# Optimization experiments

Measured on AMD Instinct MI355X. Metric: run time of the kernel, lower is better.

Reference implementation:

```python
import jax, jax.numpy as jnp
import numpy as np

EPS = 1e-5

def _ln(x, g, b):
    m = x.mean(-1, keepdims=True)
    v = jnp.var(x, axis=-1, keepdims=True)
    return (x - m) * jax.lax.rsqrt(v + EPS) * g + b

def _conv(x, w, b, stride=1, pad=1):
    y = jax.lax.conv_general_dilated(x, w, (stride, stride), [(pad, pad), (pad, pad)],
                                     dimension_numbers=('NCHW', 'OIHW', 'NCHW'))
    return y + b[None, :, None, None]

def _bn(x, g, b, m, v):
    # inference-mode BatchNorm2d
    inv = jax.lax.rsqrt(v + EPS)
    return (x - m[None, :, None, None]) * (g * inv)[None, :, None, None] + b[None, :, None, None]

def _sru_dir(u0, u1, u2, res, vf, vr, bf, br, reverse):
    # elementwise gated recurrence (SRU v2, identity activation, no dropout)
    def step(c, inp):
        a0, a1, a2, rx = inp
        f = jax.nn.sigmoid(a1 + vf * c + bf)
        c2 = f * c + (1.0 - f) * a0
        r = jax.nn.sigmoid(a2 + vr * c2 + br)
        return c2, r * c2 + (1.0 - r) * rx
    c0 = jnp.zeros_like(u0[0])
    _, hs = jax.lax.scan(step, c0, (u0, u1, u2, res), reverse=reverse)
    return hs

def _sru_layer(x, g, b, wp, w, vc, bias, k, h):
    # x: [L,B,n_in]; layer_norm on input, factored weight (projection), bidirectional
    xn = _ln(x, g, b)
    L, B, _ = xn.shape
    U = (xn @ wp) @ w                      # [L,B,2*k*h]
    U = U.reshape(L, B, 2, k, h)
    outs = []
    for d, rev in ((0, False), (1, True)):
        u = U[:, :, d]
        res = u[..., 3, :] if k == 4 else xn[..., d * h:(d + 1) * h]
        outs.append(_sru_dir(u[..., 0, :], u[..., 1, :], u[..., 2, :], res,
                             vc[d, 0], vc[d, 1], bias[d, 0], bias[d, 1], rev))
    return jnp.concatenate(outs, axis=-1)

def _forward(x, conv0_w, conv0_b, rconv1_w, rconv1_b, rbn1_g, rbn1_b, rbn1_m, rbn1_v,
             rconv2_w, rconv2_b, rbn2_g, rbn2_b, rbn2_m, rbn2_v,
             ln0_g, ln0_b, wproj0, w0, vc0, bias0, ln_g, ln_b, wproj, w, vc, bias,
             cln_g, cln_b, cls_w):
    H = 512
    h = _conv(x, conv0_w, conv0_b, stride=2)           # [B,32,F/2,T/2]
    for i in range(3):                                  # 3 residual blocks
        r = h
        h1 = jax.nn.relu(_bn(_conv(h, rconv1_w[i], rconv1_b[i]), rbn1_g[i], rbn1_b[i], rbn1_m[i], rbn1_v[i]))
        h2 = _bn(_conv(h1, rconv2_w[i], rconv2_b[i]), rbn2_g[i], rbn2_b[i], rbn2_m[i], rbn2_v[i])
        h = jax.nn.relu(h2 + r)
    Bb, C, Fr, Tt = h.shape
    s = h.reshape(Bb, C * Fr, Tt).transpose(2, 0, 1)   # [T,B,2048]
    s = _sru_layer(s, ln0_g, ln0_b, wproj0, w0, vc0, bias0, 4, H)  # layer 0: n_in != n_out -> k=4
    for i in range(3):                                  # layers 1..3: n_in == n_out -> k=3
        s = _sru_layer(s, ln_g[i], ln_b[i], wproj[i], w[i], vc[i], bias[i], 3, H)
    s = s.transpose(1, 0, 2)                            # [B,T,1024]
    s = _ln(s, cln_g, cln_b)
    return s @ cls_w                                    # [B,T,30]

def setup_inputs():
    key = jax.random.key(0)
    ks = iter(jax.random.split(key, 32))
    def nrm(shape, scale=1.0):
        return jax.random.normal(next(ks), shape, jnp.float32) * scale
    H, P, F2, D, hb = 512, 256, 2048, 1024, -2.0
    d = {}
    d['x'] = nrm((16, 1, 128, 2048))
    d['conv0_w'] = nrm((32, 1, 3, 3), (2.0 / 9) ** 0.5)
    d['conv0_b'] = jnp.zeros((32,))
    d['rconv1_w'] = nrm((3, 32, 32, 3, 3), (2.0 / (32 * 9)) ** 0.5)
    d['rconv1_b'] = jnp.zeros((3, 32))
    d['rbn1_g'] = jnp.ones((3, 32)); d['rbn1_b'] = jnp.zeros((3, 32))
    d['rbn1_m'] = nrm((3, 32), 0.1); d['rbn1_v'] = jnp.ones((3, 32))
    d['rconv2_w'] = nrm((3, 32, 32, 3, 3), (2.0 / (32 * 9)) ** 0.5)
    d['rconv2_b'] = jnp.zeros((3, 32))
    d['rbn2_g'] = 0.1 * jnp.ones((3, 32)); d['rbn2_b'] = jnp.zeros((3, 32))
    d['rbn2_m'] = nrm((3, 32), 0.1); d['rbn2_v'] = jnp.ones((3, 32))
    d['ln0_g'] = jnp.ones((F2,)); d['ln0_b'] = jnp.zeros((F2,))
    d['wproj0'] = nrm((F2, P), F2 ** -0.5)
    d['w0'] = nrm((P, 2 * 4 * H), P ** -0.5)
    d['vc0'] = nrm((2, 2, H), 0.1)
    d['bias0'] = jnp.zeros((2, 2, H)).at[:, 0].set(hb)
    d['ln_g'] = jnp.ones((3, D)); d['ln_b'] = jnp.zeros((3, D))
    d['wproj'] = nrm((3, D, P), D ** -0.5)
    d['w'] = nrm((3, P, 2 * 3 * H), P ** -0.5)
    d['vc'] = nrm((3, 2, 2, H), 0.1)
    d['bias'] = jnp.zeros((3, 2, 2, H)).at[:, :, 0].set(hb)
    d['cln_g'] = jnp.ones((D,)); d['cln_b'] = jnp.zeros((D,))
    d['cls_w'] = nrm((D, 30), D ** -0.5)
    return d

def reference(x, conv0_w, conv0_b, rconv1_w, rconv1_b, rbn1_g, rbn1_b, rbn1_m, rbn1_v,
              rconv2_w, rconv2_b, rbn2_g, rbn2_b, rbn2_m, rbn2_v,
              ln0_g, ln0_b, wproj0, w0, vc0, bias0, ln_g, ln_b, wproj, w, vc, bias,
              cln_g, cln_b, cls_w):
    return _forward(x, conv0_w, conv0_b, rconv1_w, rconv1_b, rbn1_g, rbn1_b, rbn1_m, rbn1_v,
                    rconv2_w, rconv2_b, rbn2_g, rbn2_b, rbn2_m, rbn2_v,
                    ln0_g, ln0_b, wproj0, w0, vc0, bias0, ln_g, ln_b, wproj, w, vc, bias,
                    cln_g, cln_b, cls_w)
```

## Files before the change

### kernel.cpp

```cpp
#include <hip/hip_runtime.h>
#include <hip/hip_bf16.h>
#include <math.h>

#define DEV __device__ __forceinline__

typedef __attribute__((ext_vector_type(8))) short short8;
typedef __attribute__((ext_vector_type(4))) float floatx4;

DEV float b2f_lo(unsigned u) { return __uint_as_float(u << 16); }
DEV float b2f_hi(unsigned u) { return __uint_as_float(u & 0xffff0000u); }

#if __has_builtin(__builtin_amdgcn_exp2f)
DEV float fexp2_(float x) { return __builtin_amdgcn_exp2f(x); }
#else
DEV float fexp2_(float x) { return exp2f(x); }
#endif
#if __has_builtin(__builtin_amdgcn_rcpf)
DEV float frcp_(float x) { return __builtin_amdgcn_rcpf(x); }
#else
DEV float frcp_(float x) { return 1.f / x; }
#endif

DEV void gl2lds16(const void* g, void* l) {
  __builtin_amdgcn_global_load_lds(
      (const __attribute__((address_space(1))) unsigned int*)g,
      (__attribute__((address_space(3))) unsigned int*)l, 16, 0, 0);
}

union U8 { uint4 u; __hip_bfloat16 h[8]; };

__global__ __launch_bounds__(256) void conv_stem_nhwc(const float* __restrict__ x,
    const float* __restrict__ w, const float* __restrict__ bias,
    __hip_bfloat16* __restrict__ out) {
  __shared__ float sX[3][2052];
  __shared__ float sW[288];
  __shared__ float sB[32];
  const int tid = threadIdx.x;
  const int f = blockIdx.x, n = blockIdx.y;
  const float* xb = x + (size_t)n * 262144;

  for (int i = tid; i < 1536; i += 256) {
    int r = i >> 9, c4 = i & 511;
    int fi = 2 * f - 1 + r;
    float4 v = {0.f, 0.f, 0.f, 0.f};
    if (fi >= 0 && fi < 128) v = *(const float4*)&xb[fi * 2048 + c4 * 4];
    sX[r][1 + c4 * 4 + 0] = v.x;
    sX[r][1 + c4 * 4 + 1] = v.y;
    sX[r][1 + c4 * 4 + 2] = v.z;
    sX[r][1 + c4 * 4 + 3] = v.w;
  }
  if (tid < 3) { sX[tid][0] = 0.f; sX[tid][2049] = 0.f; }
  for (int i = tid; i < 288; i += 256) sW[i] = w[i];
  if (tid < 32) sB[tid] = bias[tid];
  __syncthreads();

  float xv[4][9];
#pragma unroll
  for (int q = 0; q < 4; ++q) {
    int t = tid + q * 256;
#pragma unroll
    for (int r = 0; r < 3; ++r)
#pragma unroll
      for (int dc = 0; dc < 3; ++dc)
        xv[q][r * 3 + dc] = sX[r][2 * t + dc];
  }
#pragma unroll
  for (int ocq = 0; ocq < 4; ++ocq) {
    float wr[8][9];
#pragma unroll
    for (int oo = 0; oo < 8; ++oo)
#pragma unroll
      for (int qq = 0; qq < 9; ++qq)
        wr[oo][qq] = sW[(ocq * 8 + oo) * 9 + qq];
#pragma unroll
    for (int q = 0; q < 4; ++q) {
      U8 o;
#pragma unroll
      for (int oo = 0; oo < 8; ++oo) {
        float acc = sB[ocq * 8 + oo];
#pragma unroll
        for (int qq = 0; qq < 9; ++qq) acc = fmaf(wr[oo][qq], xv[q][qq], acc);
        o.h[oo] = __float2bfloat16(acc);
      }
      int t = tid + q * 256;
      *(uint4*)&out[(((size_t)n * 64 + f) * 1024 + t) * 32 + ocq * 8] = o.u;
    }
  }
}

__global__ __launch_bounds__(256) void wtap_conv6(const float* __restrict__ w1,
    const float* __restrict__ w2, __hip_bfloat16* __restrict__ out) {
  int i = blockIdx.x * 256 + threadIdx.x;
  if (i < 55296) {
    int b = i / 9216, r = i - b * 9216;
    int layer = b >> 1, which = b & 1;
    const float* src = (which ? w2 : w1) + layer * 9216;
    int tap = r >> 10, oc = (r >> 5) & 31, ic = r & 31;
    out[b * 9216 + r] = __float2bfloat16(src[(oc * 32 + ic) * 9 + tap]);
  }
}

template <int ADD>
__global__ __launch_bounds__(256) void conv_mfma(const __hip_bfloat16* __restrict__ Hin,
    const __hip_bfloat16* __restrict__ wt,
    const float* __restrict__ cb, const float* __restrict__ bg,
    const float* __restrict__ bb, const float* __restrict__ bm,
    const float* __restrict__ bv, __hip_bfloat16* Hres) {
  __shared__ __hip_bfloat16 sIn[6 * 130 * 40];
  __hip_bfloat16* sOut = sIn;
  const int tid = threadIdx.x;
  const int tb = blockIdx.x, fb = blockIdx.y, n = blockIdx.z;
  const int t0 = tb * 128, f0 = fb * 4;
  const __hip_bfloat16* Hb = Hin + (size_t)n * 2097152;

  for (int c = tid; c < 3120; c += 256) {
    int rr = c / 520;
    int r2 = c - rr * 520;
    int p = r2 >> 2, icq = r2 & 3;
    int fi = f0 - 1 + rr;
    int tg = t0 + p - 1;
    uint4 v = {0, 0, 0, 0};
    if (fi >= 0 && fi < 64 && tg >= 0 && tg < 1024)
      v = *(const uint4*)&Hb[((size_t)fi * 1024 + tg) * 32 + icq * 8];
    *(uint4*)&sIn[(rr * 130 + p) * 40 + icq * 8] = v;
  }

  const int lane = tid & 63, wave = tid >> 6;
  const int fr = lane & 15, fq = lane >> 4;
  short8 bfrag[9][2];
#pragma unroll
  for (int tap = 0; tap < 9; ++tap)
#pragma unroll
    for (int j = 0; j < 2; ++j)
      bfrag[tap][j] = *(const short8*)&wt[(tap * 32 + j * 16 + fr) * 32 + fq * 8];

  __syncthreads();

  const int tw = wave * 32;
  floatx4 acc[4][2][2];
#pragma unroll
  for (int fp = 0; fp < 4; ++fp)
#pragma unroll
    for (int mi = 0; mi < 2; ++mi)
#pragma unroll
      for (int j = 0; j < 2; ++j) acc[fp][mi][j] = (floatx4){0.f, 0.f, 0.f, 0.f};

#pragma unroll
  for (int fp = 0; fp < 4; ++fp) {
#pragma unroll
    for (int mi = 0; mi < 2; ++mi) {
      int pbase = tw + mi * 16 + fr;
#pragma unroll
      for (int df = 0; df < 3; ++df)
#pragma unroll
        for (int dc = 0; dc < 3; ++dc) {
          short8 af =
              *(const short8*)&sIn[((fp + df) * 130 + pbase + dc) * 40 + fq * 8];
          acc[fp][mi][0] = __builtin_amdgcn_mfma_f32_16x16x32_bf16(
              af, bfrag[df * 3 + dc][0], acc[fp][mi][0], 0, 0, 0);
          acc[fp][mi][1] = __builtin_amdgcn_mfma_f32_16x16x32_bf16(
              af, bfrag[df * 3 + dc][1], acc[fp][mi][1], 0, 0, 0);
        }
    }
  }

  float sc0 = bg[fr] * rsqrtf(bv[fr] + 1e-5f);
  float sh0 = (cb[fr] - bm[fr]) * sc0 + bb[fr];
  float sc1 = bg[fr + 16] * rsqrtf(bv[fr + 16] + 1e-5f);
  float sh1 = (cb[fr + 16] - bm[fr + 16]) * sc1 + bb[fr + 16];

  __syncthreads();
#pragma unroll
  for (int fp = 0; fp < 4; ++fp)
#pragma unroll
    for (int mi = 0; mi < 2; ++mi)
#pragma unroll
      for (int j = 0; j < 2; ++j) {
        float sc = j ? sc1 : sc0, sh = j ? sh1 : sh0;
#pragma unroll
        for (int reg = 0; reg < 4; ++reg) {
          int t_l = tw + mi * 16 + fq * 4 + reg;
          sOut[(fp * 128 + t_l) * 40 + j * 16 + fr] =
              __float2bfloat16(acc[fp][mi][j][reg] * sc + sh);
        }
      }
  __syncthreads();

  for (int c = tid; c < 2048; c += 256) {
    int fp = c >> 9, rem = c & 511;
    int t_l = rem >> 2, icq = rem & 3;
    U8 y;
    y.u = *(uint4*)&sOut[(fp * 128 + t_l) * 40 + icq * 8];
    size_t addr = (((size_t)n * 64 + f0 + fp) * 1024 + t0 + t_l) * 32 + icq * 8;
    U8 o;
    if (ADD) {
      U8 r;
      r.u = *(const uint4*)&Hres[addr];
#pragma unroll
      for (int i = 0; i < 8; ++i)
        o.h[i] = __float2bfloat16(
            fmaxf(__bfloat162float(y.h[i]) + __bfloat162float(r.h[i]), 0.f));
    } else {
#pragma unroll
      for (int i = 0; i < 8; ++i)
        o.h[i] = __float2bfloat16(fmaxf(__bfloat162float(y.h[i]), 0.f));
    }
    *(uint4*)&Hres[addr] = o.u;
  }
}

__global__ __launch_bounds__(256) void ln_nhwc(const __hip_bfloat16* __restrict__ H,
    const float* __restrict__ g, const float* __restrict__ b,
    __hip_bfloat16* __restrict__ xn) {
  int r = blockIdx.x;
  int t = r >> 4, n = r & 15;
  int tid = threadIdx.x;
  int f = tid >> 2, icq = tid & 3;
  U8 v;
  v.u = *(const uint4*)&H[(((size_t)n * 64 + f) * 1024 + t) * 32 + icq * 8];
  float xv[8];
  float sum = 0.f, ss = 0.f;
#pragma unroll
  for (int i = 0; i < 8; ++i) {
    xv[i] = __bfloat162float(v.h[i]);
    sum += xv[i];
    ss += xv[i] * xv[i];
  }
#pragma unroll
  for (int off = 32; off > 0; off >>= 1) {
    sum += __shfl_down(sum, off);
    ss  += __shfl_down(ss, off);
  }
  __shared__ float red[8];
  int lane = tid & 63, wave = tid >> 6;
  if (lane == 0) { red[wave] = sum; red[4 + wave] = ss; }
  __syncthreads();
  sum = red[0] + red[1] + red[2] + red[3];
  ss  = red[4] + red[5] + red[6] + red[7];
  float mean = sum * (1.f / 2048.f);
  float var = ss * (1.f / 2048.f) - mean * mean;
  float inv = rsqrtf(var + 1e-5f);
  U8 o;
#pragma unroll
  for (int i = 0; i < 8; ++i) {
    int cf = (icq * 8 + i) * 64 + f;
    o.h[i] = __float2bfloat16((xv[i] - mean) * inv * g[cf] + b[cf]);
  }
  *(uint4*)&xn[(size_t)r * 2048 + tid * 8] = o.u;
}

__global__ __launch_bounds__(256) void wt_perm0(const float* __restrict__ in,
    __hip_bfloat16* __restrict__ out) {
  int i = blockIdx.x * 256 + threadIdx.x;
  int p = i >> 11, kp = i & 2047;
  int ic = kp & 31, f = kp >> 5;
  out[i] = __float2bfloat16(in[(ic * 64 + f) * 256 + p]);
}

__global__ __launch_bounds__(256) void ln_rows_h(const __hip_bfloat16* __restrict__ in,
    const float* __restrict__ g, const float* __restrict__ b,
    __hip_bfloat16* __restrict__ out) {
  int r = blockIdx.x;
  int tid = threadIdx.x;
  union { ushort4 u; __hip_bfloat16 h[4]; } iv;
  iv.u = *(const ushort4*)&in[(size_t)r * 1024 + tid * 4];
  float x0 = __bfloat162float(iv.h[0]);
  float x1 = __bfloat162float(iv.h[1]);
  float x2 = __bfloat162float(iv.h[2]);
  float x3 = __bfloat162float(iv.h[3]);
  float sum = x0 + x1 + x2 + x3;
  float ss = x0 * x0 + x1 * x1 + x2 * x2 + x3 * x3;
#pragma unroll
  for (int off = 32; off > 0; off >>= 1) {
    sum += __shfl_down(sum, off);
    ss  += __shfl_down(ss, off);
  }
  __shared__ float red[8];
  int lane = tid & 63, wave = tid >> 6;
  if (lane == 0) { red[wave] = sum; red[4 + wave] = ss; }
  __syncthreads();
  sum = red[0] + red[1] + red[2] + red[3];
  ss  = red[4] + red[5] + red[6] + red[7];
  float mean = sum * (1.f / 1024.f);
  float var = ss * (1.f / 1024.f) - mean * mean;
  float inv = rsqrtf(var + 1e-5f);
  float4 gv = *(const float4*)&g[tid * 4];
  float4 bv = *(const float4*)&b[tid * 4];
  union { ushort4 u; __hip_bfloat16 h[4]; } o;
  o.h[0] = __float2bfloat16((x0 - mean) * inv * gv.x + bv.x);
  o.h[1] = __float2bfloat16((x1 - mean) * inv * gv.y + bv.y);
  o.h[2] = __float2bfloat16((x2 - mean) * inv * gv.z + bv.z);
  o.h[3] = __float2bfloat16((x3 - mean) * inv * gv.w + bv.w);
  *(ushort4*)&out[(size_t)r * 1024 + tid * 4] = o.u;
}

__global__ __launch_bounds__(256) void wt_bf16(const float* __restrict__ in,
    __hip_bfloat16* __restrict__ out, int K, int N, int inStride, int outStride) {
  __shared__ float tile[32][33];
  int x = threadIdx.x, y0 = threadIdx.y;
  int bn = blockIdx.x * 32;
  int bk = blockIdx.y * 32;
  const float* src = in + (size_t)blockIdx.z * inStride;
  __hip_bfloat16* dst = out + (size_t)blockIdx.z * outStride;
#pragma unroll
  for (int i = 0; i < 4; ++i) {
    int yy = y0 + i * 8;
    tile[yy][x] = src[(size_t)(bk + yy) * N + bn + x];
  }
  __syncthreads();
#pragma unroll
  for (int i = 0; i < 4; ++i) {
    int yy = y0 + i * 8;
    dst[(size_t)(bn + yy) * K + bk + x] = __float2bfloat16(tile[x][yy]);
  }
}

__global__ void wexp_prep(const float* __restrict__ in,
    __hip_bfloat16* __restrict__ out, int korig, int inStride, int outStride) {
  __shared__ float tile[32][33];
  int jt = blockIdx.x;
  int ckt = blockIdx.y;
  int z = blockIdx.z;
  int layer = z >> 3, dk = z & 7;
  int d = dk >> 2, k = dk & 3;
  const float* src = in + (size_t)layer * inStride;
  __hip_bfloat16* dst = out + (size_t)layer * outStride;
  int x = threadIdx.x, y0 = threadIdx.y;
  bool valid = (k < korig);
#pragma unroll
  for (int i = 0; i < 4; ++i) {
    int yy = y0 + i * 8;
    tile[yy][x] = valid
        ? src[(size_t)(ckt * 32 + yy) * (korig * 1024) + (d * korig + k) * 512 +
              jt * 32 + x]
        : 0.f;
  }
  __syncthreads();
#pragma unroll
  for (int i = 0; i < 4; ++i) {
    int yy = y0 + i * 8;
    dst[(size_t)((d * 512 + jt * 32 + yy) * 4 + k) * 256 + ckt * 32 + x] =
        __float2bfloat16(tile[x][yy]);
  }
}

__global__ __launch_bounds__(256) void wct_prep(const float* __restrict__ in,
    __hip_bfloat16* __restrict__ out) {
  int i = blockIdx.x * 256 + threadIdx.x;
  int nn = i >> 10, kk = i & 1023;
  out[i] = __float2bfloat16(nn < 30 ? in[kk * 30 + nn] : 0.f);
}

__global__ __launch_bounds__(256) void gemm_bf16(const __hip_bfloat16* __restrict__ A,
    const __hip_bfloat16* __restrict__ Bt, __hip_bfloat16* __restrict__ C,
    const __hip_bfloat16* __restrict__ xnres, int M, int N, int K) {
  __shared__ __hip_bfloat16 As[128 * 32];
  __shared__ __hip_bfloat16 Bs[128 * 32];
  const int tid = threadIdx.x;
  const int m0 = blockIdx.y * 128, n0 = blockIdx.x * 128;
  const int lane = tid & 63, wave = tid >> 6;
  const int wm = wave & 1, wn = wave >> 1;
  const int fr = lane & 15, fq = lane >> 4;
  const int srow = lane >> 2, sch = lane & 3;

  const __hip_bfloat16* ga0 = &A[(size_t)(m0 + wave * 32 + srow) * K + sch * 8];
  const __hip_bfloat16* ga1 = ga0 + (size_t)16 * K;
  const __hip_bfloat16* gb0 = &Bt[(size_t)(n0 + wave * 32 + srow) * K + sch * 8];
  const __hip_bfloat16* gb1 = gb0 + (size_t)16 * K;
  __hip_bfloat16* la0 = &As[(wave * 32) * 32];
  __hip_bfloat16* la1 = &As[(wave * 32 + 16) * 32];
  __hip_bfloat16* lb0 = &Bs[(wave * 32) * 32];
  __hip_bfloat16* lb1 = &Bs[(wave * 32 + 16) * 32];

  floatx4 acc[4][4];
#pragma unroll
  for (int i = 0; i < 4; ++i)
#pragma unroll
    for (int j = 0; j < 4; ++j)
      acc[i][j] = (floatx4){0.f, 0.f, 0.f, 0.f};

  for (int k0 = 0; k0 < K; k0 += 32) {
    __syncthreads();
    gl2lds16(ga0 + k0, la0);
    gl2lds16(ga1 + k0, la1);
    gl2lds16(gb0 + k0, lb0);
    gl2lds16(gb1 + k0, lb1);
    __syncthreads();

    short8 af[4], bf_[4];
#pragma unroll
    for (int i = 0; i < 4; ++i) {
      af[i]  = *(const short8*)&As[(wm * 64 + i * 16 + fr) * 32 + fq * 8];
      bf_[i] = *(const short8*)&Bs[(wn * 64 + i * 16 + fr) * 32 + fq * 8];
    }
#pragma unroll
    for (int i = 0; i < 4; ++i)
#pragma unroll
      for (int j = 0; j < 4; ++j)
        acc[i][j] = __builtin_amdgcn_mfma_f32_16x16x32_bf16(af[i], bf_[j],
                                                            acc[i][j], 0, 0, 0);
  }

  const bool dofuse = (xnres != nullptr);
  if (dofuse) {
    const int nq0 = n0 >> 2;
    __syncthreads();
    const __hip_bfloat16* gx =
        &xnres[(size_t)(m0 + wave * 32 + srow) * 1024 + nq0 + sch * 8];
    gl2lds16(gx, la0);
    gl2lds16(gx + (size_t)16 * 1024, la1);
    __syncthreads();
  }

#pragma unroll
  for (int i = 0; i < 4; ++i)
#pragma unroll
    for (int j = 0; j < 4; ++j)
#pragma unroll
      for (int reg = 0; reg < 4; ++reg) {
        int rloc = wm * 64 + i * 16 + fq * 4 + reg;
        int row = m0 + rloc;
        int col = n0 + wn * 64 + j * 16 + fr;
        __hip_bfloat16 val;
        if (dofuse && (fr & 3) == 3)
          val = As[rloc * 32 + wn * 16 + j * 4 + (fr >> 2)];
        else
          val = __float2bfloat16(acc[i][j][reg]);
        C[(size_t)row * N + col] = val;
      }
}

__global__ __launch_bounds__(256) void cls_gemm(const __hip_bfloat16* __restrict__ A,
    const __hip_bfloat16* __restrict__ Wct, float* __restrict__ out) {
  const int tid = threadIdx.x;
  const int lane = tid & 63, wave = tid >> 6;
  const int fr = lane & 15, fq = lane >> 4;
  const int m0 = (blockIdx.x * 4 + wave) * 16;
  floatx4 acc[2];
  acc[0] = (floatx4){0.f, 0.f, 0.f, 0.f};
  acc[1] = (floatx4){0.f, 0.f, 0.f, 0.f};
#pragma unroll 4
  for (int k0 = 0; k0 < 1024; k0 += 32) {
    short8 af = *(const short8*)&A[(size_t)(m0 + fr) * 1024 + k0 + fq * 8];
    short8 b0 = *(const short8*)&Wct[(size_t)fr * 1024 + k0 + fq * 8];
    short8 b1 = *(const short8*)&Wct[(size_t)(16 + fr) * 1024 + k0 + fq * 8];
    acc[0] = __builtin_amdgcn_mfma_f32_16x16x32_bf16(af, b0, acc[0], 0, 0, 0);
    acc[1] = __builtin_amdgcn_mfma_f32_16x16x32_bf16(af, b1, acc[1], 0, 0, 0);
  }
#pragma unroll
  for (int j = 0; j < 2; ++j) {
    int col = j * 16 + fr;
    if (col < 30) {
#pragma unroll
      for (int reg = 0; reg < 4; ++reg) {
        int row = m0 + fq * 4 + reg;
        int t = row >> 4, n = row & 15;
        out[(size_t)n * 30720 + t * 30 + col] = acc[j][reg];
      }
    }
  }
}

__global__ __launch_bounds__(64) void sru_scan(const __hip_bfloat16* __restrict__ U,
    const float* __restrict__ vc, const float* __restrict__ bias,
    __hip_bfloat16* __restrict__ out) {
  int gid = blockIdx.x * 64 + threadIdx.x;
  int j = gid & 511;
  int n = (gid >> 9) & 15;
  int d = gid >> 13;
  const float NL2E = -1.44269504f;
  float vf2 = NL2E * vc[(d * 2 + 0) * 512 + j];
  float vr2 = NL2E * vc[(d * 2 + 1) * 512 + j];
  float bf2 = NL2E * bias[(d * 2 + 0) * 512 + j];
  float br2 = NL2E * bias[(d * 2 + 1) * 512 + j];

  const char* Ub = (const char*)(U + (size_t)n * 4096 + d * 2048) + (size_t)j * 8;
  char* Ob = (char*)(out + (size_t)n * 1024 + d * 512) + (size_t)j * 2;
  const int US = d ? -131072 : 131072;
  const int OS = d ? -32768 : 32768;
  int uoff = d ? 1023 * 131072 : 0;
  int ooff = d ? 1023 * 32768 : 0;

  uint2 B0[16], B1[16], B2[16], B3[16];
  float c = 0.f;

#define LOADC(UB)                                                         \
  {                                                                       \
    _Pragma("unroll") for (int ss = 0; ss < 16; ++ss) {                   \
      UB[ss] = *(const uint2*)(Ub + uoff);                                \
      uoff += US;                                                         \
    }                                                                     \
  }

#define COMPC(UB)                                                         \
  {                                                                       \
    _Pragma("unroll") for (int ss = 0; ss < 16; ++ss) {                   \
      uint2 uv = UB[ss];                                                  \
      float a0 = b2f_lo(uv.x), a1 = b2f_hi(uv.x), a2 = b2f_lo(uv.y);      \
      float rx = b2f_hi(uv.y);                                            \
      float A1 = fmaf(a1, NL2E, bf2);                                     \
      float f = frcp_(1.f + fexp2_(fmaf(vf2, c, A1)));                    \
      float c2 = fmaf(f, c - a0, a0);                                     \
      float A2 = fmaf(a2, NL2E, br2);                                     \
      float r = frcp_(1.f + fexp2_(fmaf(vr2, c2, A2)));                   \
      float y = fmaf(r, c2 - rx, rx);                                     \
      *(__hip_bfloat16*)(Ob + ooff) = __float2bfloat16(y);                \
      ooff += OS;                                                         \
      c = c2;                                                             \
    }                                                                     \
  }

  LOADC(B0);
  LOADC(B1);
  LOADC(B2);
  for (int cb = 0; cb < 64; cb += 4) {
    LOADC(B3);
    COMPC(B0);
    if (cb + 4 < 64) LOADC(B0);
    COMPC(B1);
    if (cb + 5 < 64) LOADC(B1);
    COMPC(B2);
    if (cb + 6 < 64) LOADC(B2);
    COMPC(B3);
  }
#undef LOADC
#undef COMPC
}

extern "C" void kernel_launch(void* const* d_in, const int* in_sizes, int n_in,
                              void* d_out, int out_size, void* d_ws, size_t ws_size,
                              hipStream_t stream) {
  const float* x        = (const float*)d_in[0];
  const float* conv0_w  = (const float*)d_in[1];
  const float* conv0_b  = (const float*)d_in[2];
  const float* rconv1_w = (const float*)d_in[3];
  const float* rconv1_b = (const float*)d_in[4];
  const float* rbn1_g   = (const float*)d_in[5];
  const float* rbn1_b   = (const float*)d_in[6];
  const float* rbn1_m   = (const float*)d_in[7];
  const float* rbn1_v   = (const float*)d_in[8];
  const float* rconv2_w = (const float*)d_in[9];
  const float* rconv2_b = (const float*)d_in[10];
  const float* rbn2_g   = (const float*)d_in[11];
  const float* rbn2_b   = (const float*)d_in[12];
  const float* rbn2_m   = (const float*)d_in[13];
  const float* rbn2_v   = (const float*)d_in[14];
  const float* ln0_g    = (const float*)d_in[15];
  const float* ln0_b    = (const float*)d_in[16];
  const float* wproj0   = (const float*)d_in[17];
  const float* w0       = (const float*)d_in[18];
  const float* vc0      = (const float*)d_in[19];
  const float* bias0    = (const float*)d_in[20];
  const float* ln_g     = (const float*)d_in[21];
  const float* ln_b     = (const float*)d_in[22];
  const float* wproj    = (const float*)d_in[23];
  const float* w        = (const float*)d_in[24];
  const float* vc       = (const float*)d_in[25];
  const float* bias     = (const float*)d_in[26];
  const float* cln_g    = (const float*)d_in[27];
  const float* cln_b    = (const float*)d_in[28];
  const float* cls_w    = (const float*)d_in[29];
  float* out = (float*)d_out;

  float* Af = (float*)d_ws;
  float* Bf = Af + 33554432;
  __hip_bfloat16* Ah = (__hip_bfloat16*)Af;
  __hip_bfloat16* Bh = (__hip_bfloat16*)Bf;

  __hip_bfloat16* hA     = Ah;
  __hip_bfloat16* hB     = Bh;
  __hip_bfloat16* wt_all = Ah + 62914560;
  __hip_bfloat16* Wp0t   = Ah + 52428800;

  __hip_bfloat16* s2h  = Bh;
  __hip_bfloat16* xnc  = Bh + 16777216;
  __hip_bfloat16* xn3  = Bh + 33554432;
  __hip_bfloat16* tmp  = Bh + 50331648;
  __hip_bfloat16* W3p  = Bh + 54525952;
  __hip_bfloat16* W0p  = Bh + 57671680;
  __hip_bfloat16* Wpt3 = Bh + 58720256;
  __hip_bfloat16* xn0  = Bh;
  __hip_bfloat16* U    = Ah;
  __hip_bfloat16* Wct  = Ah;

  wtap_conv6<<<216, 256, 0, stream>>>(rconv1_w, rconv2_w, wt_all);
  wt_perm0<<<2048, 256, 0, stream>>>(wproj0, Wp0t);
  wexp_prep<<<dim3(16, 8, 8), dim3(32, 8), 0, stream>>>(w0, W0p, 4, 0, 0);
  wexp_prep<<<dim3(16, 8, 24), dim3(32, 8), 0, stream>>>(w, W3p, 3,
                                                         786432, 1048576);
  wt_bf16<<<dim3(8, 32, 3), dim3(32, 8), 0, stream>>>(wproj, Wpt3, 1024, 256,
                                                      262144, 262144);

  conv_stem_nhwc<<<dim3(64, 16), 256, 0, stream>>>(x, conv0_w, conv0_b, hA);
  for (int i = 0; i < 3; ++i) {
    conv_mfma<0><<<dim3(8, 16, 16), 256, 0, stream>>>(hA, wt_all + (i * 2) * 9216,
        rconv1_b + i * 32, rbn1_g + i * 32, rbn1_b + i * 32,
        rbn1_m + i * 32, rbn1_v + i * 32, hB);
    conv_mfma<1><<<dim3(8, 16, 16), 256, 0, stream>>>(hB, wt_all + (i * 2 + 1) * 9216,
        rconv2_b + i * 32, rbn2_g + i * 32, rbn2_b + i * 32,
        rbn2_m + i * 32, rbn2_v + i * 32, hA);
  }

  ln_nhwc<<<16384, 256, 0, stream>>>(hA, ln0_g, ln0_b, xn0);
  gemm_bf16<<<dim3(2, 128), 256, 0, stream>>>(xn0, Wp0t, tmp, nullptr,
                                              16384, 256, 2048);
  gemm_bf16<<<dim3(32, 128), 256, 0, stream>>>(tmp, W0p, U, nullptr,
                                               16384, 4096, 256);
  sru_scan<<<256, 64, 0, stream>>>(U, vc0, bias0, s2h);

  for (int i = 0; i < 3; ++i) {
    ln_rows_h<<<16384, 256, 0, stream>>>(s2h, ln_g + i * 1024, ln_b + i * 1024, xn3);
    gemm_bf16<<<dim3(2, 128), 256, 0, stream>>>(xn3, Wpt3 + i * 262144, tmp,
                                                nullptr, 16384, 256, 1024);
    gemm_bf16<<<dim3(32, 128), 256, 0, stream>>>(tmp, W3p + i * 1048576, U, xn3,
                                                 16384, 4096, 256);
    sru_scan<<<256, 64, 0, stream>>>(U, vc + i * 2048, bias + i * 2048, s2h);
  }

  ln_rows_h<<<16384, 256, 0, stream>>>(s2h, cln_g, cln_b, xnc);
  wct_prep<<<128, 256, 0, stream>>>(cls_w, Wct);
  cls_gemm<<<256, 256, 0, stream>>>(xnc, Wct, out);
}
```

Measured before the change: 1.207 ms.

## Drop padded k=4 slot in SRU layers and halve conv tile width

For the three k=3 SRU layers, the weight layout now packs only the three real gate columns: u0/u1 are interleaved and u2 sits in a separate block. The expansion GEMM therefore computes N=3072 instead of 4096, skipping the zero-padded fourth slot and the residual-fusion epilogue. A new scan kernel, sru_scan3, reads the residual directly from the layer-normed input. Separately, the residual conv kernel now uses 64-wide time tiles instead of 128 to double the block count and reduce LDS per block, at the cost of more halo reloads.

```diff
diff --git a/kernel.cpp b/kernel.cpp
--- a/kernel.cpp
+++ b/kernel.cpp
@@ -106,23 +106,23 @@
     const float* __restrict__ cb, const float* __restrict__ bg,
     const float* __restrict__ bb, const float* __restrict__ bm,
     const float* __restrict__ bv, __hip_bfloat16* Hres) {
-  __shared__ __hip_bfloat16 sIn[6 * 130 * 40];
+  __shared__ __hip_bfloat16 sIn[6 * 66 * 40];
   __hip_bfloat16* sOut = sIn;
   const int tid = threadIdx.x;
   const int tb = blockIdx.x, fb = blockIdx.y, n = blockIdx.z;
-  const int t0 = tb * 128, f0 = fb * 4;
+  const int t0 = tb * 64, f0 = fb * 4;
   const __hip_bfloat16* Hb = Hin + (size_t)n * 2097152;
 
-  for (int c = tid; c < 3120; c += 256) {
-    int rr = c / 520;
-    int r2 = c - rr * 520;
+  for (int c = tid; c < 1584; c += 256) {
+    int rr = c / 264;
+    int r2 = c - rr * 264;
     int p = r2 >> 2, icq = r2 & 3;
     int fi = f0 - 1 + rr;
     int tg = t0 + p - 1;
     uint4 v = {0, 0, 0, 0};
     if (fi >= 0 && fi < 64 && tg >= 0 && tg < 1024)
       v = *(const uint4*)&Hb[((size_t)fi * 1024 + tg) * 32 + icq * 8];
-    *(uint4*)&sIn[(rr * 130 + p) * 40 + icq * 8] = v;
+    *(uint4*)&sIn[(rr * 66 + p) * 40 + icq * 8] = v;
   }
 
   const int lane = tid & 63, wave = tid >> 6;
@@ -136,32 +136,27 @@
 
   __syncthreads();
 
-  const int tw = wave * 32;
-  floatx4 acc[4][2][2];
+  const int tw = wave * 16;
+  floatx4 acc[4][2];
 #pragma unroll
   for (int fp = 0; fp < 4; ++fp)
 #pragma unroll
-    for (int mi = 0; mi < 2; ++mi)
-#pragma unroll
-      for (int j = 0; j < 2; ++j) acc[fp][mi][j] = (floatx4){0.f, 0.f, 0.f, 0.f};
+    for (int j = 0; j < 2; ++j) acc[fp][j] = (floatx4){0.f, 0.f, 0.f, 0.f};
 
 #pragma unroll
   for (int fp = 0; fp < 4; ++fp) {
-#pragma unroll
-    for (int mi = 0; mi < 2; ++mi) {
-      int pbase = tw + mi * 16 + fr;
-#pragma unroll
-      for (int df = 0; df < 3; ++df)
-#pragma unroll
-        for (int dc = 0; dc < 3; ++dc) {
-          short8 af =
-              *(const short8*)&sIn[((fp + df) * 130 + pbase + dc) * 40 + fq * 8];
-          acc[fp][mi][0] = __builtin_amdgcn_mfma_f32_16x16x32_bf16(
-              af, bfrag[df * 3 + dc][0], acc[fp][mi][0], 0, 0, 0);
-          acc[fp][mi][1] = __builtin_amdgcn_mfma_f32_16x16x32_bf16(
-              af, bfrag[df * 3 + dc][1], acc[fp][mi][1], 0, 0, 0);
-        }
-    }
+    int pbase = tw + fr;
+#pragma unroll
+    for (int df = 0; df < 3; ++df)
+#pragma unroll
+      for (int dc = 0; dc < 3; ++dc) {
+        short8 af =
+            *(const short8*)&sIn[((fp + df) * 66 + pbase + dc) * 40 + fq * 8];
+        acc[fp][0] = __builtin_amdgcn_mfma_f32_16x16x32_bf16(
+            af, bfrag[df * 3 + dc][0], acc[fp][0], 0, 0, 0);
+        acc[fp][1] = __builtin_amdgcn_mfma_f32_16x16x32_bf16(
+            af, bfrag[df * 3 + dc][1], acc[fp][1], 0, 0, 0);
+      }
   }
 
   float sc0 = bg[fr] * rsqrtf(bv[fr] + 1e-5f);
@@ -173,24 +168,22 @@
 #pragma unroll
   for (int fp = 0; fp < 4; ++fp)
 #pragma unroll
-    for (int mi = 0; mi < 2; ++mi)
-#pragma unroll
-      for (int j = 0; j < 2; ++j) {
-        float sc = j ? sc1 : sc0, sh = j ? sh1 : sh0;
-#pragma unroll
-        for (int reg = 0; reg < 4; ++reg) {
-          int t_l = tw + mi * 16 + fq * 4 + reg;
-          sOut[(fp * 128 + t_l) * 40 + j * 16 + fr] =
-              __float2bfloat16(acc[fp][mi][j][reg] * sc + sh);
-        }
+    for (int j = 0; j < 2; ++j) {
+      float sc = j ? sc1 : sc0, sh = j ? sh1 : sh0;
+#pragma unroll
+      for (int reg = 0; reg < 4; ++reg) {
+        int t_l = tw + fq * 4 + reg;
+        sOut[(fp * 64 + t_l) * 40 + j * 16 + fr] =
+            __float2bfloat16(acc[fp][j][reg] * sc + sh);
       }
-  __syncthreads();
-
-  for (int c = tid; c < 2048; c += 256) {
-    int fp = c >> 9, rem = c & 511;
+    }
+  __syncthreads();
+
+  for (int c = tid; c < 1024; c += 256) {
+    int fp = c >> 8, rem = c & 255;
     int t_l = rem >> 2, icq = rem & 3;
     U8 y;
-    y.u = *(uint4*)&sOut[(fp * 128 + t_l) * 40 + icq * 8];
+    y.u = *(uint4*)&sOut[(fp * 64 + t_l) * 40 + icq * 8];
     size_t addr = (((size_t)n * 64 + f0 + fp) * 1024 + t0 + t_l) * 32 + icq * 8;
     U8 o;
     if (ADD) {
@@ -323,24 +316,27 @@
   int z = blockIdx.z;
   int layer = z >> 3, dk = z & 7;
   int d = dk >> 2, k = dk & 3;
+  if (k >= korig) return;
   const float* src = in + (size_t)layer * inStride;
   __hip_bfloat16* dst = out + (size_t)layer * outStride;
   int x = threadIdx.x, y0 = threadIdx.y;
-  bool valid = (k < korig);
 #pragma unroll
   for (int i = 0; i < 4; ++i) {
     int yy = y0 + i * 8;
-    tile[yy][x] = valid
-        ? src[(size_t)(ckt * 32 + yy) * (korig * 1024) + (d * korig + k) * 512 +
-              jt * 32 + x]
-        : 0.f;
+    tile[yy][x] = src[(size_t)(ckt * 32 + yy) * (korig * 1024) +
+                      (d * korig + k) * 512 + jt * 32 + x];
   }
   __syncthreads();
 #pragma unroll
   for (int i = 0; i < 4; ++i) {
     int yy = y0 + i * 8;
-    dst[(size_t)((d * 512 + jt * 32 + yy) * 4 + k) * 256 + ckt * 32 + x] =
-        __float2bfloat16(tile[x][yy]);
+    int j = jt * 32 + yy;
+    int rIdx;
+    if (korig == 4)
+      rIdx = (d * 512 + j) * 4 + k;
+    else
+      rIdx = (k < 2) ? ((d * 512 + j) * 2 + k) : (2048 + d * 512 + j);
+    dst[(size_t)rIdx * 256 + ckt * 32 + x] = __float2bfloat16(tile[x][yy]);
   }
 }
 
@@ -353,7 +349,7 @@
 
 __global__ __launch_bounds__(256) void gemm_bf16(const __hip_bfloat16* __restrict__ A,
     const __hip_bfloat16* __restrict__ Bt, __hip_bfloat16* __restrict__ C,
-    const __hip_bfloat16* __restrict__ xnres, int M, int N, int K) {
+    int M, int N, int K) {
   __shared__ __hip_bfloat16 As[128 * 32];
   __shared__ __hip_bfloat16 Bs[128 * 32];
   const int tid = threadIdx.x;
@@ -401,32 +397,15 @@
                                                             acc[i][j], 0, 0, 0);
   }
 
-  const bool dofuse = (xnres != nullptr);
-  if (dofuse) {
-    const int nq0 = n0 >> 2;
-    __syncthreads();
-    const __hip_bfloat16* gx =
-        &xnres[(size_t)(m0 + wave * 32 + srow) * 1024 + nq0 + sch * 8];
-    gl2lds16(gx, la0);
-    gl2lds16(gx + (size_t)16 * 1024, la1);
-    __syncthreads();
-  }
-
 #pragma unroll
   for (int i = 0; i < 4; ++i)
 #pragma unroll
     for (int j = 0; j < 4; ++j)
 #pragma unroll
       for (int reg = 0; reg < 4; ++reg) {
-        int rloc = wm * 64 + i * 16 + fq * 4 + reg;
-        int row = m0 + rloc;
+        int row = m0 + wm * 64 + i * 16 + fq * 4 + reg;
         int col = n0 + wn * 64 + j * 16 + fr;
-        __hip_bfloat16 val;
-        if (dofuse && (fr & 3) == 3)
-          val = As[rloc * 32 + wn * 16 + j * 4 + (fr >> 2)];
-        else
-          val = __float2bfloat16(acc[i][j][reg]);
-        C[(size_t)row * N + col] = val;
+        C[(size_t)row * N + col] = __float2bfloat16(acc[i][j][reg]);
       }
 }
 
@@ -461,7 +440,7 @@
   }
 }
 
-__global__ __launch_bounds__(64) void sru_scan(const __hip_bfloat16* __restrict__ U,
+__global__ __launch_bounds__(64) void sru_scan4(const __hip_bfloat16* __restrict__ U,
     const float* __restrict__ vc, const float* __restrict__ bias,
     __hip_bfloat16* __restrict__ out) {
   int gid = blockIdx.x * 64 + threadIdx.x;
@@ -522,6 +501,85 @@
     COMPC(B2);
     if (cb + 6 < 64) LOADC(B2);
     COMPC(B3);
+  }
+#undef LOADC
+#undef COMPC
+}
+
+__global__ __launch_bounds__(64) void sru_scan3(const __hip_bfloat16* __restrict__ U,
+    const __hip_bfloat16* __restrict__ xn,
+    const float* __restrict__ vc, const float* __restrict__ bias,
+    __hip_bfloat16* __restrict__ out) {
+  int gid = blockIdx.x * 64 + threadIdx.x;
+  int j = gid & 511;
+  int n = (gid >> 9) & 15;
+  int d = gid >> 13;
+  const float NL2E = -1.44269504f;
+  float vf2 = NL2E * vc[(d * 2 + 0) * 512 + j];
+  float vr2 = NL2E * vc[(d * 2 + 1) * 512 + j];
+  float bf2 = NL2E * bias[(d * 2 + 0) * 512 + j];
+  float br2 = NL2E * bias[(d * 2 + 1) * 512 + j];
+
+  const char* Ub01 = (const char*)U + (size_t)n * 6144 + (size_t)(d * 512 + j) * 4;
+  const char* Ub2  = (const char*)U + (size_t)n * 6144 +
+                     (size_t)(2048 + d * 512 + j) * 2;
+  const char* Xb = (const char*)xn + (size_t)n * 2048 + (size_t)(d * 512 + j) * 2;
+  char* Ob = (char*)(out + (size_t)n * 1024 + d * 512) + (size_t)j * 2;
+  const int US = d ? -98304 : 98304;
+  const int XS = d ? -32768 : 32768;
+  const int OS = d ? -32768 : 32768;
+  int uoff = d ? 1023 * 98304 : 0;
+  int u2off = uoff;
+  int xoff = d ? 1023 * 32768 : 0;
+  int ooff = xoff;
+
+  uint B0u[16], B1u[16], B2u[16], B3u[16];
+  ushort B0a[16], B1a[16], B2a[16], B3a[16];
+  ushort B0x[16], B1x[16], B2x[16], B3x[16];
+  float c = 0.f;
+
+#define LOADC(Bu, Ba, Bx)                                                 \
+  {                                                                       \
+    _Pragma("unroll") for (int ss = 0; ss < 16; ++ss) {                   \
+      Bu[ss] = *(const uint*)(Ub01 + uoff);                               \
+      Ba[ss] = *(const ushort*)(Ub2 + u2off);                             \
+      Bx[ss] = *(const ushort*)(Xb + xoff);                               \
+      uoff += US;                                                         \
+      u2off += US;                                                        \
+      xoff += XS;                                                         \
+    }                                                                     \
+  }
+
+#define COMPC(Bu, Ba, Bx)                                                 \
+  {                                                                       \
+    _Pragma("unroll") for (int ss = 0; ss < 16; ++ss) {                   \
+      float a0 = b2f_lo(Bu[ss]), a1 = b2f_hi(Bu[ss]);                     \
+      float a2 = __uint_as_float((uint)Ba[ss] << 16);                     \
+      float rx = __uint_as_float((uint)Bx[ss] << 16);                     \
+      float A1 = fmaf(a1, NL2E, bf2);                                     \
+      float f = frcp_(1.f + fexp2_(fmaf(vf2, c, A1)));                    \
+      float c2 = fmaf(f, c - a0, a0);                                     \
+      float A2 = fmaf(a2, NL2E, br2);                                     \
+      float r = frcp_(1.f + fexp2_(fmaf(vr2, c2, A2)));                   \
+      float y = fmaf(r, c2 - rx, rx);                                     \
+      *(__hip_bfloat16*)(Ob + ooff) = __float2bfloat16(y);                \
+      ooff += OS;                                                         \
+      c = c2;                                                             \
+    }                                                                     \
+  }
+
+  LOADC(B0u, B0a, B0x);
+  LOADC(B1u, B1a, B1x);
+  LOADC(B2u, B2a, B2x);
+  for (int cb = 0; cb < 64; cb += 4) {
+    LOADC(B3u, B3a, B3x);
+    COMPC(B0u, B0a, B0x);
+    if (cb + 4 < 64) LOADC(B0u, B0a, B0x);
+    COMPC(B1u, B1a, B1x);
+    if (cb + 5 < 64) LOADC(B1u, B1a, B1x);
+    COMPC(B2u, B2a, B2x);
+    if (cb + 6 < 64) LOADC(B2u, B2a, B2x);
+    COMPC(B3u, B3a, B3x);
   }
 #undef LOADC
 #undef COMPC
@@ -587,34 +645,32 @@
   wt_perm0<<<2048, 256, 0, stream>>>(wproj0, Wp0t);
   wexp_prep<<<dim3(16, 8, 8), dim3(32, 8), 0, stream>>>(w0, W0p, 4, 0, 0);
   wexp_prep<<<dim3(16, 8, 24), dim3(32, 8), 0, stream>>>(w, W3p, 3,
-                                                         786432, 1048576);
+                                                         786432, 786432);
   wt_bf16<<<dim3(8, 32, 3), dim3(32, 8), 0, stream>>>(wproj, Wpt3, 1024, 256,
                                                       262144, 262144);
 
   conv_stem_nhwc<<<dim3(64, 16), 256, 0, stream>>>(x, conv0_w, conv0_b, hA);
   for (int i = 0; i < 3; ++i) {
-    conv_mfma<0><<<dim3(8, 16, 16), 256, 0, stream>>>(hA, wt_all + (i * 2) * 9216,
+    conv_mfma<0><<<dim3(16, 16, 16), 256, 0, stream>>>(hA, wt_all + (i * 2) * 9216,
         rconv1_b + i * 32, rbn1_g + i * 32, rbn1_b + i * 32,
         rbn1_m + i * 32, rbn1_v + i * 32, hB);
-    conv_mfma<1><<<dim3(8, 16, 16), 256, 0, stream>>>(hB, wt_all + (i * 2 + 1) * 9216,
+    conv_mfma<1><<<dim3(16, 16, 16), 256, 0, stream>>>(hB, wt_all + (i * 2 + 1) * 9216,
         rconv2_b + i * 32, rbn2_g + i * 32, rbn2_b + i * 32,
         rbn2_m + i * 32, rbn2_v + i * 32, hA);
   }
 
   ln_nhwc<<<16384, 256, 0, stream>>>(hA, ln0_g, ln0_b, xn0);
-  gemm_bf16<<<dim3(2, 128), 256, 0, stream>>>(xn0, Wp0t, tmp, nullptr,
-                                              16384, 256, 2048);
-  gemm_bf16<<<dim3(32, 128), 256, 0, stream>>>(tmp, W0p, U, nullptr,
-                                               16384, 4096, 256);
-  sru_scan<<<256, 64, 0, stream>>>(U, vc0, bias0, s2h);
+  gemm_bf16<<<dim3(2, 128), 256, 0, stream>>>(xn0, Wp0t, tmp, 16384, 256, 2048);
+  gemm_bf16<<<dim3(32, 128), 256, 0, stream>>>(tmp, W0p, U, 16384, 4096, 256);
+  sru_scan4<<<256, 64, 0, stream>>>(U, vc0, bias0, s2h);
 
   for (int i = 0; i < 3; ++i) {
     ln_rows_h<<<16384, 256, 0, stream>>>(s2h, ln_g + i * 1024, ln_b + i * 1024, xn3);
     gemm_bf16<<<dim3(2, 128), 256, 0, stream>>>(xn3, Wpt3 + i * 262144, tmp,
-                                                nullptr, 16384, 256, 1024);
-    gemm_bf16<<<dim3(32, 128), 256, 0, stream>>>(tmp, W3p + i * 1048576, U, xn3,
-                                                 16384, 4096, 256);
-    sru_scan<<<256, 64, 0, stream>>>(U, vc + i * 2048, bias + i * 2048, s2h);
+                                                16384, 256, 1024);
+    gemm_bf16<<<dim3(24, 128), 256, 0, stream>>>(tmp, W3p + i * 786432, U,
+                                                 16384, 3072, 256);
+    sru_scan3<<<256, 64, 0, stream>>>(U, xn3, vc + i * 2048, bias + i * 2048, s2h);
   }
 
   ln_rows_h<<<16384, 256, 0, stream>>>(s2h, cln_g, cln_b, xnc);
```

After: 1.166 ms. 3.4% less time.
